# Optimization experiments

Hardware: AMD Instinct MI355X
Metric: run time of the kernel (lower is better)

The kernel has to match this reference:

```python
import jax, jax.numpy as jnp
import numpy as np

N_NODES = 100000
N_EDGES = 800000
D = 128   # latent feature width (node & edge)
H = 128   # MLP hidden width


def setup_inputs() -> dict:
    key = jax.random.key(0)
    ks = jax.random.split(key, 8)
    w = lambda k, shape: jax.random.normal(k, shape, jnp.float32) * 0.05
    return {
        "node_features": jax.random.normal(ks[0], (N_NODES, D), jnp.float32),
        "edge_features": jax.random.normal(ks[1], (N_EDGES, D), jnp.float32),
        "senders": jax.random.randint(ks[2], (N_EDGES,), 0, N_NODES),
        "receivers": jax.random.randint(ks[3], (N_EDGES,), 0, N_NODES),
        "We1": w(ks[4], (3 * D, H)), "be1": jnp.zeros((H,), jnp.float32),
        "We2": w(ks[5], (H, D)),     "be2": jnp.zeros((D,), jnp.float32),
        "Wn1": w(ks[6], (2 * D, H)), "bn1": jnp.zeros((H,), jnp.float32),
        "Wn2": w(ks[7], (H, D)),     "bn2": jnp.zeros((D,), jnp.float32),
    }


def _mlp(x, W1, b1, W2, b2):
    return jax.nn.relu(x @ W1 + b1) @ W2 + b2


def reference(node_features, edge_features, senders, receivers,
              We1, be1, We2, be2, Wn1, bn1, Wn2, bn2):
    # --- edge update: gather sender/receiver node feats, concat, MLP ---
    e_in = jnp.concatenate(
        [node_features[senders], node_features[receivers], edge_features], axis=-1
    )  # [E, 3D]
    e_upd = _mlp(e_in, We1, be1, We2, be2)  # [E, D]

    # --- node update: scatter-sum updated edge feats to receivers, concat, MLP ---
    agg = jax.ops.segment_sum(e_upd, receivers, num_segments=node_features.shape[0])
    n_in = jnp.concatenate([node_features, agg], axis=-1)  # [N, 2D]
    n_upd = _mlp(n_in, Wn1, bn1, Wn2, bn2)  # [N, D]

    # --- residuals ---
    new_nodes = node_features + n_upd
    new_edges = edge_features + e_upd
    return new_nodes, new_edges
```

## Files before the change

kernel.cpp:

```cpp
#include <hip/hip_runtime.h>
#include <hip/hip_bf16.h>
#include <stdint.h>

#define D 128
#define NNODES 100000
#define NEDGES 800000
#define LDSTR 136

typedef __bf16 bf16_t;
typedef bf16_t bf16x8 __attribute__((ext_vector_type(8)));
typedef float  f32x4  __attribute__((ext_vector_type(4)));

__global__ void wprep_kernel(const float* __restrict__ src, bf16_t* __restrict__ dst,
                             int K, int N) {
  int idx = blockIdx.x * blockDim.x + threadIdx.x;
  if (idx >= K * N) return;
  int n = idx / K;
  int k = idx - n * K;
  dst[idx] = (bf16_t)src[(size_t)k * N + n];
}

__global__ __launch_bounds__(256) void edge_kernel(
    const float* __restrict__ node_f, const float* __restrict__ edge_f,
    const int* __restrict__ senders, const int* __restrict__ receivers,
    const bf16_t* __restrict__ W1T,
    const float* __restrict__ be1,
    const bf16_t* __restrict__ W2T,
    const float* __restrict__ be2,
    float* __restrict__ agg,
    float* __restrict__ out_edges)
{
  __shared__ bf16_t As[128 * LDSTR];
  __shared__ int s_snd[128];
  __shared__ int s_rcv[128];

  const int tid  = threadIdx.x;
  const int base = blockIdx.x * 128;

  if (tid < 128) s_snd[tid] = senders[base + tid];
  else           s_rcv[tid - 128] = receivers[base + tid - 128];

  const int lane = tid & 63;
  const int wave = tid >> 6;
  const int q    = lane >> 4;
  const int ln   = lane & 15;
  const int m0   = (wave & 1) * 64;
  const int n0   = (wave >> 1) * 64;

  f32x4 acc[4][4];
  #pragma unroll
  for (int i = 0; i < 4; i++)
    #pragma unroll
    for (int j = 0; j < 4; j++) acc[i][j] = {0.f, 0.f, 0.f, 0.f};

  const int sr = tid >> 1;
  const int sc = (tid & 1) * 64;

  __syncthreads();

  for (int c = 0; c < 3; ++c) {
    const float* src;
    if (c == 0)      src = node_f + (size_t)s_snd[sr] * D;
    else if (c == 1) src = node_f + (size_t)s_rcv[sr] * D;
    else             src = edge_f + (size_t)(base + sr) * D;
    #pragma unroll
    for (int v = 0; v < 8; ++v) {
      float4 f0 = ((const float4*)src)[(sc >> 2) + 2 * v];
      float4 f1 = ((const float4*)src)[(sc >> 2) + 2 * v + 1];
      bf16x8 b = {(bf16_t)f0.x, (bf16_t)f0.y, (bf16_t)f0.z, (bf16_t)f0.w,
                  (bf16_t)f1.x, (bf16_t)f1.y, (bf16_t)f1.z, (bf16_t)f1.w};
      *(bf16x8*)&As[sr * LDSTR + sc + v * 8] = b;
    }
    __syncthreads();
    #pragma unroll
    for (int kk = 0; kk < 128; kk += 32) {
      bf16x8 a[4], bb[4];
      #pragma unroll
      for (int i = 0; i < 4; i++)
        a[i] = *(const bf16x8*)&As[(m0 + i * 16 + ln) * LDSTR + kk + q * 8];
      const int kg = c * 128 + kk + q * 8;
      #pragma unroll
      for (int j = 0; j < 4; j++)
        bb[j] = *(const bf16x8*)&W1T[(size_t)(n0 + j * 16 + ln) * 384 + kg];
      #pragma unroll
      for (int i = 0; i < 4; i++)
        #pragma unroll
        for (int j = 0; j < 4; j++)
          acc[i][j] = __builtin_amdgcn_mfma_f32_16x16x32_bf16(a[i], bb[j], acc[i][j], 0, 0, 0);
    }
    __syncthreads();
  }

  #pragma unroll
  for (int i = 0; i < 4; i++)
    #pragma unroll
    for (int j = 0; j < 4; j++)
      #pragma unroll
      for (int r = 0; r < 4; r++) {
        int row = m0 + i * 16 + q * 4 + r;
        int col = n0 + j * 16 + ln;
        float v = acc[i][j][r] + be1[col];
        As[row * LDSTR + col] = (bf16_t)fmaxf(v, 0.f);
      }
  __syncthreads();

  f32x4 acc2[4][4];
  #pragma unroll
  for (int i = 0; i < 4; i++)
    #pragma unroll
    for (int j = 0; j < 4; j++) acc2[i][j] = {0.f, 0.f, 0.f, 0.f};

  #pragma unroll
  for (int kk = 0; kk < 128; kk += 32) {
    bf16x8 a[4], bb[4];
    #pragma unroll
    for (int i = 0; i < 4; i++)
      a[i] = *(const bf16x8*)&As[(m0 + i * 16 + ln) * LDSTR + kk + q * 8];
    #pragma unroll
    for (int j = 0; j < 4; j++)
      bb[j] = *(const bf16x8*)&W2T[(size_t)(n0 + j * 16 + ln) * 128 + kk + q * 8];
    #pragma unroll
    for (int i = 0; i < 4; i++)
      #pragma unroll
      for (int j = 0; j < 4; j++)
        acc2[i][j] = __builtin_amdgcn_mfma_f32_16x16x32_bf16(a[i], bb[j], acc2[i][j], 0, 0, 0);
  }

  #pragma unroll
  for (int i = 0; i < 4; i++)
    #pragma unroll
    for (int j = 0; j < 4; j++)
      #pragma unroll
      for (int r = 0; r < 4; r++) {
        int row = m0 + i * 16 + q * 4 + r;
        int col = n0 + j * 16 + ln;
        float v = acc2[i][j][r] + be2[col];
        size_t e = (size_t)(base + row);
        out_edges[e * D + col] = edge_f[e * D + col] + v;
        unsafeAtomicAdd(&agg[(size_t)s_rcv[row] * D + col], v);
      }
}

__global__ __launch_bounds__(256) void node_kernel(
    const float* __restrict__ node_f,
    const bf16_t* __restrict__ W1T,
    const float* __restrict__ b1,
    const bf16_t* __restrict__ W2T,
    const float* __restrict__ b2,
    const float* __restrict__ agg,
    float* __restrict__ out_nodes)
{
  __shared__ bf16_t As[128 * LDSTR];

  const int tid    = threadIdx.x;
  const int base   = blockIdx.x * 128;
  const int nvalid = min(128, NNODES - base);

  const int lane = tid & 63;
  const int wave = tid >> 6;
  const int q    = lane >> 4;
  const int ln   = lane & 15;
  const int m0   = (wave & 1) * 64;
  const int n0   = (wave >> 1) * 64;

  f32x4 acc[4][4];
  #pragma unroll
  for (int i = 0; i < 4; i++)
    #pragma unroll
    for (int j = 0; j < 4; j++) acc[i][j] = {0.f, 0.f, 0.f, 0.f};

  const int sr = tid >> 1;
  const int sc = (tid & 1) * 64;
  const size_t src_row = (size_t)(base + min(sr, nvalid - 1));

  for (int c = 0; c < 2; ++c) {
    const float* src = (c == 0 ? node_f : agg) + src_row * D;
    #pragma unroll
    for (int v = 0; v < 8; ++v) {
      float4 f0 = ((const float4*)src)[(sc >> 2) + 2 * v];
      float4 f1 = ((const float4*)src)[(sc >> 2) + 2 * v + 1];
      bf16x8 b = {(bf16_t)f0.x, (bf16_t)f0.y, (bf16_t)f0.z, (bf16_t)f0.w,
                  (bf16_t)f1.x, (bf16_t)f1.y, (bf16_t)f1.z, (bf16_t)f1.w};
      *(bf16x8*)&As[sr * LDSTR + sc + v * 8] = b;
    }
    __syncthreads();
    #pragma unroll
    for (int kk = 0; kk < 128; kk += 32) {
      bf16x8 a[4], bb[4];
      #pragma unroll
      for (int i = 0; i < 4; i++)
        a[i] = *(const bf16x8*)&As[(m0 + i * 16 + ln) * LDSTR + kk + q * 8];
      const int kg = c * 128 + kk + q * 8;
      #pragma unroll
      for (int j = 0; j < 4; j++)
        bb[j] = *(const bf16x8*)&W1T[(size_t)(n0 + j * 16 + ln) * 256 + kg];
      #pragma unroll
      for (int i = 0; i < 4; i++)
        #pragma unroll
        for (int j = 0; j < 4; j++)
          acc[i][j] = __builtin_amdgcn_mfma_f32_16x16x32_bf16(a[i], bb[j], acc[i][j], 0, 0, 0);
    }
    __syncthreads();
  }

  #pragma unroll
  for (int i = 0; i < 4; i++)
    #pragma unroll
    for (int j = 0; j < 4; j++)
      #pragma unroll
      for (int r = 0; r < 4; r++) {
        int row = m0 + i * 16 + q * 4 + r;
        int col = n0 + j * 16 + ln;
        float v = acc[i][j][r] + b1[col];
        As[row * LDSTR + col] = (bf16_t)fmaxf(v, 0.f);
      }
  __syncthreads();

  f32x4 acc2[4][4];
  #pragma unroll
  for (int i = 0; i < 4; i++)
    #pragma unroll
    for (int j = 0; j < 4; j++) acc2[i][j] = {0.f, 0.f, 0.f, 0.f};

  #pragma unroll
  for (int kk = 0; kk < 128; kk += 32) {
    bf16x8 a[4], bb[4];
    #pragma unroll
    for (int i = 0; i < 4; i++)
      a[i] = *(const bf16x8*)&As[(m0 + i * 16 + ln) * LDSTR + kk + q * 8];
    #pragma unroll
    for (int j = 0; j < 4; j++)
      bb[j] = *(const bf16x8*)&W2T[(size_t)(n0 + j * 16 + ln) * 128 + kk + q * 8];
    #pragma unroll
    for (int i = 0; i < 4; i++)
      #pragma unroll
      for (int j = 0; j < 4; j++)
        acc2[i][j] = __builtin_amdgcn_mfma_f32_16x16x32_bf16(a[i], bb[j], acc2[i][j], 0, 0, 0);
  }

  #pragma unroll
  for (int i = 0; i < 4; i++)
    #pragma unroll
    for (int j = 0; j < 4; j++)
      #pragma unroll
      for (int r = 0; r < 4; r++) {
        int row = m0 + i * 16 + q * 4 + r;
        if (row < nvalid) {
          int col = n0 + j * 16 + ln;
          float v = acc2[i][j][r] + b2[col];
          size_t nidx = (size_t)(base + row);
          out_nodes[nidx * D + col] = node_f[nidx * D + col] + v;
        }
      }
}

extern "C" void kernel_launch(void* const* d_in, const int* in_sizes, int n_in,
                              void* d_out, int out_size, void* d_ws, size_t ws_size,
                              hipStream_t stream) {
  const float* node_f    = (const float*)d_in[0];
  const float* edge_f    = (const float*)d_in[1];
  const int*   senders   = (const int*)d_in[2];
  const int*   receivers = (const int*)d_in[3];
  const float* We1 = (const float*)d_in[4];
  const float* be1 = (const float*)d_in[5];
  const float* We2 = (const float*)d_in[6];
  const float* be2 = (const float*)d_in[7];
  const float* Wn1 = (const float*)d_in[8];
  const float* bn1 = (const float*)d_in[9];
  const float* Wn2 = (const float*)d_in[10];
  const float* bn2 = (const float*)d_in[11];

  float* out_nodes = (float*)d_out;
  float* out_edges = out_nodes + (size_t)NNODES * D;

  bf16_t* W1T  = (bf16_t*)d_ws;
  bf16_t* W2T  = W1T  + 128 * 384;
  bf16_t* Wn1T = W2T  + 128 * 128;
  bf16_t* Wn2T = Wn1T + 128 * 256;

  hipMemsetAsync(d_out, 0, (size_t)NNODES * D * sizeof(float), stream);

  wprep_kernel<<<(384 * 128 + 255) / 256, 256, 0, stream>>>(We1, W1T, 384, 128);
  wprep_kernel<<<(128 * 128 + 255) / 256, 256, 0, stream>>>(We2, W2T, 128, 128);
  wprep_kernel<<<(256 * 128 + 255) / 256, 256, 0, stream>>>(Wn1, Wn1T, 256, 128);
  wprep_kernel<<<(128 * 128 + 255) / 256, 256, 0, stream>>>(Wn2, Wn2T, 128, 128);

  edge_kernel<<<NEDGES / 128, 256, 0, stream>>>(
      node_f, edge_f, senders, receivers, W1T, be1, W2T, be2, out_nodes, out_edges);

  node_kernel<<<(NNODES + 127) / 128, 256, 0, stream>>>(
      node_f, Wn1T, bn1, Wn2T, bn2, out_nodes, out_nodes);
}
```

Before: 1.475 ms.

## Load MFMA A-operands directly from global memory and stage residual epilogue through LDS

The first-layer A operands are now read straight from global memory (gathered node rows and edge rows) into registers and converted to bf16 per MFMA step. This removes the LDS staging pass and its barriers. The residual output write goes through an LDS transpose so the edge/node features are read and written as coalesced float4 rows, replacing scattered scalar accesses. Launch bounds now request 3 blocks per CU, and bias and receiver index loads are hoisted out of the epilogue loop. The cost is redundant global reads of A rows across the two column-waves, plus extra register pressure.

Measured after the change: 1.414 ms. 1.04x faster.

```diff
diff --git a/kernel.cpp b/kernel.cpp
--- a/kernel.cpp
+++ b/kernel.cpp
@@ -6,6 +6,7 @@
 #define NNODES 100000
 #define NEDGES 800000
 #define LDSTR 136
+#define EFSTR 132
 
 typedef __bf16 bf16_t;
 typedef bf16_t bf16x8 __attribute__((ext_vector_type(8)));
@@ -20,7 +21,31 @@
   dst[idx] = (bf16_t)src[(size_t)k * N + n];
 }
 
-__global__ __launch_bounds__(256) void edge_kernel(
+#define MFMA_CHUNK(AP, WPTR, WS, CB) do {                                        \
+    _Pragma("unroll")                                                            \
+    for (int kk = 0; kk < 128; kk += 32) {                                       \
+      bf16x8 a[4], bb[4];                                                        \
+      _Pragma("unroll")                                                          \
+      for (int i = 0; i < 4; ++i) {                                              \
+        float4 f0 = *(const float4*)((AP)[i] + kk + q * 8);                      \
+        float4 f1 = *(const float4*)((AP)[i] + kk + q * 8 + 4);                  \
+        a[i] = (bf16x8){(bf16_t)f0.x, (bf16_t)f0.y, (bf16_t)f0.z, (bf16_t)f0.w, \
+                        (bf16_t)f1.x, (bf16_t)f1.y, (bf16_t)f1.z, (bf16_t)f1.w};\
+      }                                                                          \
+      const int kg = (CB) + kk + q * 8;                                          \
+      _Pragma("unroll")                                                          \
+      for (int j = 0; j < 4; ++j)                                                \
+        bb[j] = *(const bf16x8*)&(WPTR)[(size_t)(n0 + j * 16 + ln) * (WS) + kg]; \
+      _Pragma("unroll")                                                          \
+      for (int i = 0; i < 4; ++i)                                                \
+        _Pragma("unroll")                                                        \
+        for (int j = 0; j < 4; ++j)                                              \
+          acc[i][j] = __builtin_amdgcn_mfma_f32_16x16x32_bf16(a[i], bb[j],       \
+                                                              acc[i][j], 0, 0, 0);\
+    }                                                                            \
+  } while (0)
+
+__global__ __launch_bounds__(256, 3) void edge_kernel(
     const float* __restrict__ node_f, const float* __restrict__ edge_f,
     const int* __restrict__ senders, const int* __restrict__ receivers,
     const bf16_t* __restrict__ W1T,
@@ -30,16 +55,10 @@
     float* __restrict__ agg,
     float* __restrict__ out_edges)
 {
-  __shared__ bf16_t As[128 * LDSTR];
-  __shared__ int s_snd[128];
-  __shared__ int s_rcv[128];
+  __shared__ __align__(16) bf16_t Hs[128 * LDSTR];
 
   const int tid  = threadIdx.x;
   const int base = blockIdx.x * 128;
-
-  if (tid < 128) s_snd[tid] = senders[base + tid];
-  else           s_rcv[tid - 128] = receivers[base + tid - 128];
-
   const int lane = tid & 63;
   const int wave = tid >> 6;
   const int q    = lane >> 4;
@@ -47,49 +66,26 @@
   const int m0   = (wave & 1) * 64;
   const int n0   = (wave >> 1) * 64;
 
+  const float* apA[4];
+  const float* apB[4];
+  const float* apC[4];
+  #pragma unroll
+  for (int i = 0; i < 4; ++i) {
+    const int row = base + m0 + i * 16 + ln;
+    apA[i] = node_f + (size_t)senders[row]   * D;
+    apB[i] = node_f + (size_t)receivers[row] * D;
+    apC[i] = edge_f + (size_t)row            * D;
+  }
+
   f32x4 acc[4][4];
   #pragma unroll
   for (int i = 0; i < 4; i++)
     #pragma unroll
     for (int j = 0; j < 4; j++) acc[i][j] = {0.f, 0.f, 0.f, 0.f};
 
-  const int sr = tid >> 1;
-  const int sc = (tid & 1) * 64;
-
-  __syncthreads();
-
-  for (int c = 0; c < 3; ++c) {
-    const float* src;
-    if (c == 0)      src = node_f + (size_t)s_snd[sr] * D;
-    else if (c == 1) src = node_f + (size_t)s_rcv[sr] * D;
-    else             src = edge_f + (size_t)(base + sr) * D;
-    #pragma unroll
-    for (int v = 0; v < 8; ++v) {
-      float4 f0 = ((const float4*)src)[(sc >> 2) + 2 * v];
-      float4 f1 = ((const float4*)src)[(sc >> 2) + 2 * v + 1];
-      bf16x8 b = {(bf16_t)f0.x, (bf16_t)f0.y, (bf16_t)f0.z, (bf16_t)f0.w,
-                  (bf16_t)f1.x, (bf16_t)f1.y, (bf16_t)f1.z, (bf16_t)f1.w};
-      *(bf16x8*)&As[sr * LDSTR + sc + v * 8] = b;
-    }
-    __syncthreads();
-    #pragma unroll
-    for (int kk = 0; kk < 128; kk += 32) {
-      bf16x8 a[4], bb[4];
-      #pragma unroll
-      for (int i = 0; i < 4; i++)
-        a[i] = *(const bf16x8*)&As[(m0 + i * 16 + ln) * LDSTR + kk + q * 8];
-      const int kg = c * 128 + kk + q * 8;
-      #pragma unroll
-      for (int j = 0; j < 4; j++)
-        bb[j] = *(const bf16x8*)&W1T[(size_t)(n0 + j * 16 + ln) * 384 + kg];
-      #pragma unroll
-      for (int i = 0; i < 4; i++)
-        #pragma unroll
-        for (int j = 0; j < 4; j++)
-          acc[i][j] = __builtin_amdgcn_mfma_f32_16x16x32_bf16(a[i], bb[j], acc[i][j], 0, 0, 0);
-    }
-    __syncthreads();
-  }
+  MFMA_CHUNK(apA, W1T, 384, 0);
+  MFMA_CHUNK(apB, W1T, 384, 128);
+  MFMA_CHUNK(apC, W1T, 384, 256);
 
   #pragma unroll
   for (int i = 0; i < 4; i++)
@@ -100,7 +96,7 @@
         int row = m0 + i * 16 + q * 4 + r;
         int col = n0 + j * 16 + ln;
         float v = acc[i][j][r] + be1[col];
-        As[row * LDSTR + col] = (bf16_t)fmaxf(v, 0.f);
+        Hs[row * LDSTR + col] = (bf16_t)fmaxf(v, 0.f);
       }
   __syncthreads();
 
@@ -115,7 +111,7 @@
     bf16x8 a[4], bb[4];
     #pragma unroll
     for (int i = 0; i < 4; i++)
-      a[i] = *(const bf16x8*)&As[(m0 + i * 16 + ln) * LDSTR + kk + q * 8];
+      a[i] = *(const bf16x8*)&Hs[(m0 + i * 16 + ln) * LDSTR + kk + q * 8];
     #pragma unroll
     for (int j = 0; j < 4; j++)
       bb[j] = *(const bf16x8*)&W2T[(size_t)(n0 + j * 16 + ln) * 128 + kk + q * 8];
@@ -126,22 +122,59 @@
         acc2[i][j] = __builtin_amdgcn_mfma_f32_16x16x32_bf16(a[i], bb[j], acc2[i][j], 0, 0, 0);
   }
 
+  float be2v[4];
+  #pragma unroll
+  for (int j = 0; j < 4; ++j) be2v[j] = be2[n0 + j * 16 + ln];
+
+  int rq[4][4];
+  #pragma unroll
+  for (int i = 0; i < 4; ++i)
+    #pragma unroll
+    for (int r = 0; r < 4; ++r)
+      rq[i][r] = receivers[base + m0 + i * 16 + q * 4 + r];
+
   #pragma unroll
   for (int i = 0; i < 4; i++)
     #pragma unroll
     for (int j = 0; j < 4; j++)
       #pragma unroll
       for (int r = 0; r < 4; r++) {
-        int row = m0 + i * 16 + q * 4 + r;
-        int col = n0 + j * 16 + ln;
-        float v = acc2[i][j][r] + be2[col];
-        size_t e = (size_t)(base + row);
-        out_edges[e * D + col] = edge_f[e * D + col] + v;
-        unsafeAtomicAdd(&agg[(size_t)s_rcv[row] * D + col], v);
+        float v = acc2[i][j][r] + be2v[j];
+        acc2[i][j][r] = v;
+        unsafeAtomicAdd(&agg[(size_t)rq[i][r] * D + n0 + j * 16 + ln], v);
       }
+
+  float* Ef = (float*)Hs;
+  const int lr = tid >> 2;
+  const int cb = (tid & 3) * 32;
+  #pragma unroll
+  for (int half = 0; half < 2; ++half) {
+    __syncthreads();
+    if (m0 == half * 64) {
+      #pragma unroll
+      for (int i = 0; i < 4; i++)
+        #pragma unroll
+        for (int j = 0; j < 4; j++)
+          #pragma unroll
+          for (int r = 0; r < 4; r++)
+            Ef[(i * 16 + q * 4 + r) * EFSTR + n0 + j * 16 + ln] = acc2[i][j][r];
+    }
+    __syncthreads();
+    const size_t grow = (size_t)(base + half * 64 + lr);
+    const float4* ep = (const float4*)(edge_f + grow * D + cb);
+    float4*       op = (float4*)(out_edges + grow * D + cb);
+    #pragma unroll
+    for (int t = 0; t < 8; ++t) {
+      float4 e = ep[t];
+      float4 v = *(const float4*)&Ef[lr * EFSTR + cb + 4 * t];
+      float4 o;
+      o.x = e.x + v.x; o.y = e.y + v.y; o.z = e.z + v.z; o.w = e.w + v.w;
+      op[t] = o;
+    }
+  }
 }
 
-__global__ __launch_bounds__(256) void node_kernel(
+__global__ __launch_bounds__(256, 3) void node_kernel(
     const float* __restrict__ node_f,
     const bf16_t* __restrict__ W1T,
     const float* __restrict__ b1,
@@ -150,7 +183,7 @@
     const float* __restrict__ agg,
     float* __restrict__ out_nodes)
 {
-  __shared__ bf16_t As[128 * LDSTR];
+  __shared__ __align__(16) bf16_t Hs[128 * LDSTR];
 
   const int tid    = threadIdx.x;
   const int base   = blockIdx.x * 128;
@@ -163,45 +196,23 @@
   const int m0   = (wave & 1) * 64;
   const int n0   = (wave >> 1) * 64;
 
+  const float* apA[4];
+  const float* apB[4];
+  #pragma unroll
+  for (int i = 0; i < 4; ++i) {
+    const size_t row = (size_t)(base + min(m0 + i * 16 + ln, nvalid - 1));
+    apA[i] = node_f + row * D;
+    apB[i] = agg    + row * D;
+  }
+
   f32x4 acc[4][4];
   #pragma unroll
   for (int i = 0; i < 4; i++)
     #pragma unroll
     for (int j = 0; j < 4; j++) acc[i][j] = {0.f, 0.f, 0.f, 0.f};
 
-  const int sr = tid >> 1;
-  const int sc = (tid & 1) * 64;
-  const size_t src_row = (size_t)(base + min(sr, nvalid - 1));
-
-  for (int c = 0; c < 2; ++c) {
-    const float* src = (c == 0 ? node_f : agg) + src_row * D;
-    #pragma unroll
-    for (int v = 0; v < 8; ++v) {
-      float4 f0 = ((const float4*)src)[(sc >> 2) + 2 * v];
-      float4 f1 = ((const float4*)src)[(sc >> 2) + 2 * v + 1];
-      bf16x8 b = {(bf16_t)f0.x, (bf16_t)f0.y, (bf16_t)f0.z, (bf16_t)f0.w,
-                  (bf16_t)f1.x, (bf16_t)f1.y, (bf16_t)f1.z, (bf16_t)f1.w};
-      *(bf16x8*)&As[sr * LDSTR + sc + v * 8] = b;
-    }
-    __syncthreads();
-    #pragma unroll
-    for (int kk = 0; kk < 128; kk += 32) {
-      bf16x8 a[4], bb[4];
-      #pragma unroll
-      for (int i = 0; i < 4; i++)
-        a[i] = *(const bf16x8*)&As[(m0 + i * 16 + ln) * LDSTR + kk + q * 8];
-      const int kg = c * 128 + kk + q * 8;
-      #pragma unroll
-      for (int j = 0; j < 4; j++)
-        bb[j] = *(const bf16x8*)&W1T[(size_t)(n0 + j * 16 + ln) * 256 + kg];
-      #pragma unroll
-      for (int i = 0; i < 4; i++)
-        #pragma unroll
-        for (int j = 0; j < 4; j++)
-          acc[i][j] = __builtin_amdgcn_mfma_f32_16x16x32_bf16(a[i], bb[j], acc[i][j], 0, 0, 0);
-    }
-    __syncthreads();
-  }
+  MFMA_CHUNK(apA, W1T, 256, 0);
+  MFMA_CHUNK(apB, W1T, 256, 128);
 
   #pragma unroll
   for (int i = 0; i < 4; i++)
@@ -212,7 +223,7 @@
         int row = m0 + i * 16 + q * 4 + r;
         int col = n0 + j * 16 + ln;
         float v = acc[i][j][r] + b1[col];
-        As[row * LDSTR + col] = (bf16_t)fmaxf(v, 0.f);
+        Hs[row * LDSTR + col] = (bf16_t)fmaxf(v, 0.f);
       }
   __syncthreads();
 
@@ -227,7 +238,7 @@
     bf16x8 a[4], bb[4];
     #pragma unroll
     for (int i = 0; i < 4; i++)
-      a[i] = *(const bf16x8*)&As[(m0 + i * 16 + ln) * LDSTR + kk + q * 8];
+      a[i] = *(const bf16x8*)&Hs[(m0 + i * 16 + ln) * LDSTR + kk + q * 8];
     #pragma unroll
     for (int j = 0; j < 4; j++)
       bb[j] = *(const bf16x8*)&W2T[(size_t)(n0 + j * 16 + ln) * 128 + kk + q * 8];
@@ -238,20 +249,46 @@
         acc2[i][j] = __builtin_amdgcn_mfma_f32_16x16x32_bf16(a[i], bb[j], acc2[i][j], 0, 0, 0);
   }
 
-  #pragma unroll
-  for (int i = 0; i < 4; i++)
-    #pragma unroll
-    for (int j = 0; j < 4; j++)
-      #pragma unroll
-      for (int r = 0; r < 4; r++) {
-        int row = m0 + i * 16 + q * 4 + r;
-        if (row < nvalid) {
-          int col = n0 + j * 16 + ln;
-          float v = acc2[i][j][r] + b2[col];
-          size_t nidx = (size_t)(base + row);
-          out_nodes[nidx * D + col] = node_f[nidx * D + col] + v;
-        }
+  float b2v[4];
+  #pragma unroll
+  for (int j = 0; j < 4; ++j) b2v[j] = b2[n0 + j * 16 + ln];
+  #pragma unroll
+  for (int i = 0; i < 4; i++)
+    #pragma unroll
+    for (int j = 0; j < 4; j++)
+      #pragma unroll
+      for (int r = 0; r < 4; r++) acc2[i][j][r] += b2v[j];
+
+  float* Ef = (float*)Hs;
+  const int lr = tid >> 2;
+  const int cb = (tid & 3) * 32;
+  #pragma unroll
+  for (int half = 0; half < 2; ++half) {
+    __syncthreads();
+    if (m0 == half * 64) {
+      #pragma unroll
+      for (int i = 0; i < 4; i++)
+        #pragma unroll
+        for (int j = 0; j < 4; j++)
+          #pragma unroll
+          for (int r = 0; r < 4; r++)
+            Ef[(i * 16 + q * 4 + r) * EFSTR + n0 + j * 16 + ln] = acc2[i][j][r];
+    }
+    __syncthreads();
+    const size_t grow = (size_t)(base + half * 64 + lr);
+    if (grow < NNODES) {
+      const float4* np = (const float4*)(node_f + grow * D + cb);
+      float4*       op = (float4*)(out_nodes + grow * D + cb);
+      #pragma unroll
+      for (int t = 0; t < 8; ++t) {
+        float4 n = np[t];
+        float4 v = *(const float4*)&Ef[lr * EFSTR + cb + 4 * t];
+        float4 o;
+        o.x = n.x + v.x; o.y = n.y + v.y; o.z = n.z + v.z; o.w = n.w + v.w;
+        op[t] = o;
       }
+    }
+  }
 }
 
 extern "C" void kernel_launch(void* const* d_in, const int* in_sizes, int n_in,
```
